# Optimization experiments

Measured on AMD Instinct MI355X. Metric: run time of the kernel, lower is better.

## Reference

```python
import jax, jax.numpy as jnp
import numpy as np

TEMPERATURE = 1.0
EPS = 1e-08


def setup_inputs() -> dict:
    key = jax.random.key(0)
    k1, k2, k3, k4 = jax.random.split(key, 4)
    B, S, D = 4, 4096, 512
    x = jax.random.normal(k1, (B, S, D), dtype=jnp.float32)
    mask = jax.random.randint(k2, (B, S), 0, 2).astype(bool)
    # nn.Linear(dim, dim): weight [out, in], bias [out]
    W = jax.random.normal(k3, (D, D), dtype=jnp.float32) * (1.0 / np.sqrt(D))
    b = jax.random.normal(k4, (D,), dtype=jnp.float32) * 0.01
    return {"x": x, "mask": mask, "W": W, "b": b}


def reference(x, mask, W, b):
    # pairwise squared euclidean distances (cdist p=2, squared)
    sq = jnp.sum(x * x, axis=-1)                                  # [B,S]
    d2 = sq[:, :, None] + sq[:, None, :] - 2.0 * jnp.einsum('bsd,btd->bst', x, x)
    d2 = jnp.maximum(d2, 0.0)                                      # [B,S,S]
    # gaussian kernel: exp(-(sqrt(d2)/T)^2) == exp(-d2/T^2) (avoids sqrt-at-0)
    w = jnp.exp(-d2 / (TEMPERATURE * TEMPERATURE))
    pair_mask = (mask[:, None, :] & mask[:, :, None]).astype(w.dtype)
    w = w * pair_mask
    denom = jnp.maximum(jnp.sum(w, axis=-1, keepdims=True), EPS)
    attn = w / denom                                               # [B,S,S]
    v = jnp.einsum('bsd,ed->bse', x, W) + b                        # [B,S,D]
    return jnp.einsum('bst,btd->bsd', attn, v)
```

## Files before the change

### kernel.cpp

```cpp
#include <hip/hip_runtime.h>
#include <hip/hip_bf16.h>
#include <stdint.h>

#define TB 4
#define TS 4096
#define TD 512
#define TN (TB*TS)

#define KS 64
#define TRI 528
#define D2_THRESH 40.0f
#define EPSV 1e-8f
#define ROW_CAP 16
#define OVF_CAP 32768

typedef unsigned short u16;
typedef unsigned int   u32;
typedef __attribute__((ext_vector_type(8))) short bf16x8;
typedef __attribute__((ext_vector_type(4))) float f32x4;

#define OFF_WH    (33554432u)
#define OFF_WL    (OFF_WH + 524288u)
#define OFF_SQ    (OFF_WL + 524288u)
#define OFF_DEN   (OFF_SQ + 65536u)
#define OFF_RC    (OFF_DEN + 65536u)
#define OFF_OC    (OFF_RC + 65536u)
#define OFF_OVF   (OFF_OC + 256u)
#define OFF_RL    (OFF_OVF + 262144u)
#define OFF_SQ64  (OFF_RL + 1048576u)

__device__ inline u16 b16(float v) {
  __hip_bfloat16 hb = __float2bfloat16(v);
  return *(u16*)&hb;
}
__device__ inline void bsplit(float v, u16& h, u16& l) {
  __hip_bfloat16 hb = __float2bfloat16(v);
  float hf = __bfloat162float(hb);
  __hip_bfloat16 lb = __float2bfloat16(v - hf);
  h = *(u16*)&hb; l = *(u16*)&lb;
}

__device__ inline void gl_lds16(const void* g, void* l) {
  __builtin_amdgcn_global_load_lds(
      (const __attribute__((address_space(1))) u32*)g,
      (__attribute__((address_space(3))) u32*)l, 16, 0, 0);
}

__global__ __launch_bounds__(256) void prep_kernel(
    const float* __restrict__ x, const float* __restrict__ W,
    u16* __restrict__ xb, float* __restrict__ sq, float* __restrict__ sq64,
    u16* __restrict__ Wh, u16* __restrict__ Wl) {
  int bid = blockIdx.x, tid = threadIdx.x;
  if (bid < TN/4) {
    int row  = bid*4 + (tid >> 6);
    int lane = tid & 63;
    const float4* xv = (const float4*)(x + (size_t)row*TD + lane*8);
    float4 a = xv[0], b = xv[1];
    float p = a.x*a.x + a.y*a.y + a.z*a.z + a.w*a.w
            + b.x*b.x + b.y*b.y + b.z*b.z + b.w*b.w;
    if (lane < 8) {
      uint4 pk;
      pk.x = (unsigned)b16(a.x) | ((unsigned)b16(a.y) << 16);
      pk.y = (unsigned)b16(a.z) | ((unsigned)b16(a.w) << 16);
      pk.z = (unsigned)b16(b.x) | ((unsigned)b16(b.y) << 16);
      pk.w = (unsigned)b16(b.z) | ((unsigned)b16(b.w) << 16);
      *(uint4*)(xb + (size_t)row*KS + lane*8) = pk;
    }
    p += __shfl_xor(p, 1); p += __shfl_xor(p, 2); p += __shfl_xor(p, 4);
    float p8 = p;
    p += __shfl_xor(p, 8); p += __shfl_xor(p, 16); p += __shfl_xor(p, 32);
    if (lane == 0) { sq[row] = p; sq64[row] = p8; }
  } else {
    int idx = (bid - TN/4)*256 + tid;
    const float4* wv = (const float4*)(W + (size_t)idx*8);
    float4 a = wv[0], b = wv[1];
    float ev[8] = {a.x,a.y,a.z,a.w,b.x,b.y,b.z,b.w};
    u16 hs[8], ls[8];
    #pragma unroll
    for (int t = 0; t < 8; ++t) bsplit(ev[t], hs[t], ls[t]);
    uint4 hv, lv;
    hv.x = hs[0]|((unsigned)hs[1]<<16); hv.y = hs[2]|((unsigned)hs[3]<<16);
    hv.z = hs[4]|((unsigned)hs[5]<<16); hv.w = hs[6]|((unsigned)hs[7]<<16);
    lv.x = ls[0]|((unsigned)ls[1]<<16); lv.y = ls[2]|((unsigned)ls[3]<<16);
    lv.z = ls[4]|((unsigned)ls[5]<<16); lv.w = ls[6]|((unsigned)ls[7]<<16);
    *(uint4*)(Wh + (size_t)idx*8) = hv;
    *(uint4*)(Wl + (size_t)idx*8) = lv;
  }
}

__device__ inline void append_pair(int gi, int gj, int* rowcnt, int* rowlist,
                                   int2* ovf, int* ovf_cnt) {
  int slot = atomicAdd(&rowcnt[gi], 1);
  if (slot < ROW_CAP) rowlist[gi*ROW_CAP + slot] = gj;
  else { int o = atomicAdd(ovf_cnt, 1); if (o < OVF_CAP) ovf[o] = make_int2(gi, gj); }
}

__global__ __launch_bounds__(256,4) void screen_kernel(
    const u16* __restrict__ xb, const float* __restrict__ sq64,
    const int* __restrict__ mask, int* __restrict__ rowcnt, int* __restrict__ rowlist,
    int2* __restrict__ ovf, int* __restrict__ ovf_cnt) {
  __shared__ __align__(16) u16 lA[128*64];
  __shared__ __align__(16) u16 lB[128*64];
  int bid = blockIdx.x;
  int batch = bid / TRI;
  int t = bid - batch*TRI;
  int ti = (int)((sqrtf(8.0f*t + 1.0f) - 1.0f)*0.5f);
  while ((ti+1)*(ti+2)/2 <= t) ++ti;
  while (ti*(ti+1)/2 > t)      --ti;
  int tj = t - ti*(ti+1)/2;
  int tid = threadIdx.x, lane = tid & 63, w = tid >> 6, wr = w >> 1, wc = w & 1;
  int rowA = batch*TS + ti*128;
  int rowB = batch*TS + tj*128;
  f32x4 zero = {0.f,0.f,0.f,0.f};
  f32x4 acc[4][4];
  #pragma unroll
  for (int m = 0; m < 4; ++m)
    #pragma unroll
    for (int n = 0; n < 4; ++n) acc[m][n] = zero;

  #pragma unroll
  for (int q = 0; q < 4; ++q) {
    int rbase = w*32 + q*8;
    int r  = rbase + (lane >> 3);
    int sg = (lane & 7) ^ (r & 7);
    gl_lds16(xb + (size_t)(rowA + r)*KS + sg*8, &lA[rbase*64]);
    gl_lds16(xb + (size_t)(rowB + r)*KS + sg*8, &lB[rbase*64]);
  }
  __syncthreads();
  #pragma unroll
  for (int kc = 0; kc < 2; ++kc) {
    bf16x8 af[4], bfr[4];
    #pragma unroll
    for (int m = 0; m < 4; ++m) {
      int r = wr*64 + m*16 + (lane & 15);
      int s0 = (lane >> 4) + kc*4;
      af[m] = *(bf16x8*)&lA[r*64 + (s0 ^ (r & 7))*8];
    }
    #pragma unroll
    for (int n = 0; n < 4; ++n) {
      int r = wc*64 + n*16 + (lane & 15);
      int s0 = (lane >> 4) + kc*4;
      bfr[n] = *(bf16x8*)&lB[r*64 + (s0 ^ (r & 7))*8];
    }
    #pragma unroll
    for (int m = 0; m < 4; ++m)
      #pragma unroll
      for (int n = 0; n < 4; ++n)
        acc[m][n] = __builtin_amdgcn_mfma_f32_16x16x32_bf16(af[m], bfr[n], acc[m][n], 0, 0, 0);
  }
  int hi = lane >> 4, lo = lane & 15;
  #pragma unroll
  for (int m = 0; m < 4; ++m) {
    #pragma unroll
    for (int n = 0; n < 4; ++n) {
      #pragma unroll
      for (int r4 = 0; r4 < 4; ++r4) {
        int gi = rowA + wr*64 + m*16 + hi*4 + r4;
        int gj = rowB + wc*64 + n*16 + lo;
        float d2 = sq64[gi] + sq64[gj] - 2.0f*acc[m][n][r4];
        if (d2 <= D2_THRESH && mask[gi] && mask[gj]) {
          append_pair(gi, gj, rowcnt, rowlist, ovf, ovf_cnt);
          if (ti != tj) append_pair(gj, gi, rowcnt, rowlist, ovf, ovf_cnt);
        }
      }
    }
  }
}

__device__ inline void accum_pair(int j, const float* __restrict__ x,
                                  const float* __restrict__ sq, float sqi,
                                  const float4& a0, const float4& a1, int lane,
                                  float acc[8], float& dsum) {
  const float4* xj = (const float4*)(x + (size_t)j*TD + lane*8);
  float4 b0 = xj[0], b1 = xj[1];
  float d = a0.x*b0.x + a0.y*b0.y + a0.z*b0.z + a0.w*b0.w
          + a1.x*b1.x + a1.y*b1.y + a1.z*b1.z + a1.w*b1.w;
  d += __shfl_xor(d, 1); d += __shfl_xor(d, 2); d += __shfl_xor(d, 4);
  d += __shfl_xor(d, 8); d += __shfl_xor(d, 16); d += __shfl_xor(d, 32);
  float d2  = fmaxf(sqi + sq[j] - 2.0f*d, 0.0f);
  float wgt = expf(-d2);
  acc[0] += wgt*b0.x; acc[1] += wgt*b0.y; acc[2] += wgt*b0.z; acc[3] += wgt*b0.w;
  acc[4] += wgt*b1.x; acc[5] += wgt*b1.y; acc[6] += wgt*b1.z; acc[7] += wgt*b1.w;
  dsum += wgt;
}

__global__ __launch_bounds__(256) void row_kernel(
    const float* __restrict__ x, const float* __restrict__ sq,
    const int* __restrict__ rowcnt, const int* __restrict__ rowlist,
    const int2* __restrict__ ovf, const int* __restrict__ ovf_cnt,
    u16* __restrict__ yh, float* __restrict__ den) {
  int i    = blockIdx.x*4 + (threadIdx.x >> 6);
  int lane = threadIdx.x & 63;
  const float4* xi = (const float4*)(x + (size_t)i*TD + lane*8);
  float4 a0 = xi[0], a1 = xi[1];
  float sqi = sq[i];
  float acc[8] = {0.f,0.f,0.f,0.f,0.f,0.f,0.f,0.f};
  float dsum = 0.f;
  int nj = rowcnt[i]; if (nj > ROW_CAP) nj = ROW_CAP;
  for (int t = 0; t < nj; ++t)
    accum_pair(rowlist[i*ROW_CAP + t], x, sq, sqi, a0, a1, lane, acc, dsum);
  int no = *ovf_cnt; if (no > OVF_CAP) no = OVF_CAP;
  for (int t = 0; t < no; ++t) {
    int2 pr = ovf[t];
    if (pr.x == i) accum_pair(pr.y, x, sq, sqi, a0, a1, lane, acc, dsum);
  }
  float inv = 1.0f / fmaxf(dsum, EPSV);
  u16 hs[8];
  #pragma unroll
  for (int e = 0; e < 8; ++e) hs[e] = b16(acc[e]*inv);
  uint4 hv;
  hv.x = hs[0]|((unsigned)hs[1]<<16); hv.y = hs[2]|((unsigned)hs[3]<<16);
  hv.z = hs[4]|((unsigned)hs[5]<<16); hv.w = hs[6]|((unsigned)hs[7]<<16);
  *(uint4*)(yh + (size_t)i*TD + lane*8) = hv;
  if (lane == 0) den[i] = dsum;
}

__global__ __launch_bounds__(256,2) void out_gemm_kernel(
    const u16* __restrict__ yh, const float* __restrict__ den,
    const u16* __restrict__ Wh, const u16* __restrict__ Wl,
    const float* __restrict__ bias, float* __restrict__ out) {
  __shared__ __align__(16) u16 lAh[128*64];
  __shared__ __align__(16) u16 lBh[128*64];
  __shared__ __align__(16) u16 lBl[128*64];
  int mt = blockIdx.x, nt = blockIdx.y;
  int tid = threadIdx.x, lane = tid & 63, w = tid >> 6, wr = w >> 1, wc = w & 1;
  f32x4 zero = {0.f,0.f,0.f,0.f};
  f32x4 acc[4][4];
  #pragma unroll
  for (int m = 0; m < 4; ++m)
    #pragma unroll
    for (int n = 0; n < 4; ++n) acc[m][n] = zero;

  for (int ks = 0; ks < 8; ++ks) {
    int k0 = ks*64;
    #pragma unroll
    for (int q = 0; q < 4; ++q) {
      int rbase = w*32 + q*8;
      int r  = rbase + (lane >> 3);
      int sg = (lane & 7) ^ (r & 7);
      size_t aoff = (size_t)(mt*128 + r)*TD + k0 + sg*8;
      size_t boff = (size_t)(nt*128 + r)*TD + k0 + sg*8;
      gl_lds16(yh + aoff, &lAh[rbase*64]);
      gl_lds16(Wh + boff, &lBh[rbase*64]);
      gl_lds16(Wl + boff, &lBl[rbase*64]);
    }
    __syncthreads();
    #pragma unroll
    for (int kc = 0; kc < 2; ++kc) {
      bf16x8 ah[4], bh[4], bl[4];
      #pragma unroll
      for (int m = 0; m < 4; ++m) {
        int r = wr*64 + m*16 + (lane & 15);
        int s0 = (lane >> 4) + kc*4;
        ah[m] = *(bf16x8*)&lAh[r*64 + (s0 ^ (r & 7))*8];
      }
      #pragma unroll
      for (int n = 0; n < 4; ++n) {
        int r = wc*64 + n*16 + (lane & 15);
        int s0 = (lane >> 4) + kc*4;
        int o = r*64 + (s0 ^ (r & 7))*8;
        bh[n] = *(bf16x8*)&lBh[o];
        bl[n] = *(bf16x8*)&lBl[o];
      }
      #pragma unroll
      for (int m = 0; m < 4; ++m)
        #pragma unroll
        for (int n = 0; n < 4; ++n) {
          acc[m][n] = __builtin_amdgcn_mfma_f32_16x16x32_bf16(ah[m], bh[n], acc[m][n], 0, 0, 0);
          acc[m][n] = __builtin_amdgcn_mfma_f32_16x16x32_bf16(ah[m], bl[n], acc[m][n], 0, 0, 0);
        }
    }
    __syncthreads();
  }
  int hi = lane >> 4, lo = lane & 15;
  #pragma unroll
  for (int m = 0; m < 4; ++m)
    #pragma unroll
    for (int n = 0; n < 4; ++n)
      #pragma unroll
      for (int r4 = 0; r4 < 4; ++r4) {
        int grow = mt*128 + wr*64 + m*16 + hi*4 + r4;
        int col  = nt*128 + wc*64 + n*16 + lo;
        float dn = den[grow];
        float s  = dn / fmaxf(dn, EPSV);
        out[(size_t)grow*TD + col] = acc[m][n][r4] + s*bias[col];
      }
}

extern "C" void kernel_launch(void* const* d_in, const int* in_sizes, int n_in,
                              void* d_out, int out_size, void* d_ws, size_t ws_size,
                              hipStream_t stream) {
  (void)in_sizes; (void)n_in; (void)out_size; (void)ws_size;
  const float* x    = (const float*)d_in[0];
  const int*   mask = (const int*)d_in[1];
  const float* W    = (const float*)d_in[2];
  const float* bias = (const float*)d_in[3];
  float* out = (float*)d_out;
  char*  ws  = (char*)d_ws;

  u16*   xb      = (u16*)(ws + 0);
  u16*   yh      = (u16*)(ws + 0);
  u16*   Wh      = (u16*)(ws + OFF_WH);
  u16*   Wl      = (u16*)(ws + OFF_WL);
  float* sq      = (float*)(ws + OFF_SQ);
  float* den     = (float*)(ws + OFF_DEN);
  int*   rowcnt  = (int*)(ws + OFF_RC);
  int*   ovf_cnt = (int*)(ws + OFF_OC);
  int2*  ovf     = (int2*)(ws + OFF_OVF);
  int*   rowlist = (int*)(ws + OFF_RL);
  float* sq64    = (float*)(ws + OFF_SQ64);

  hipMemsetAsync(rowcnt, 0, 65536 + 256, stream);
  prep_kernel<<<TN/4 + 128, 256, 0, stream>>>(x, W, xb, sq, sq64, Wh, Wl);
  screen_kernel<<<TB*TRI, 256, 0, stream>>>(xb, sq64, mask, rowcnt, rowlist, ovf, ovf_cnt);
  row_kernel<<<TN/4, 256, 0, stream>>>(x, sq, rowcnt, rowlist, ovf, ovf_cnt, yh, den);
  dim3 g(TN/128, TD/128);
  out_gemm_kernel<<<g, 256, 0, stream>>>(yh, den, Wh, Wl, bias, out);
}
```

Measured before the change: 139.7 us.

## Drop W low-part split GEMM, fold mask into sq64, and remove memset

The output GEMM now multiplies by a single bf16 copy of W instead of the high+low split, which halves its MFMAs and its LDS and global traffic for B. That also allows four blocks per CU instead of two. The mask is folded into sq64 as a huge sentinel, so screening no longer reads the mask, and the memset of the counters is merged into prep_kernel. The bias load in the epilogue is hoisted. W now contributes only bf16 precision to the output, which raises error and could matter for tolerance.

```diff
diff --git a/kernel.cpp b/kernel.cpp
--- a/kernel.cpp
+++ b/kernel.cpp
@@ -13,6 +13,7 @@
 #define EPSV 1e-8f
 #define ROW_CAP 16
 #define OVF_CAP 32768
+#define MASKED_SQ 1e30f
 
 typedef unsigned short u16;
 typedef unsigned int   u32;
@@ -33,12 +34,6 @@
   __hip_bfloat16 hb = __float2bfloat16(v);
   return *(u16*)&hb;
 }
-__device__ inline void bsplit(float v, u16& h, u16& l) {
-  __hip_bfloat16 hb = __float2bfloat16(v);
-  float hf = __bfloat162float(hb);
-  __hip_bfloat16 lb = __float2bfloat16(v - hf);
-  h = *(u16*)&hb; l = *(u16*)&lb;
-}
 
 __device__ inline void gl_lds16(const void* g, void* l) {
   __builtin_amdgcn_global_load_lds(
@@ -48,9 +43,11 @@
 
 __global__ __launch_bounds__(256) void prep_kernel(
     const float* __restrict__ x, const float* __restrict__ W,
+    const int* __restrict__ mask,
     u16* __restrict__ xb, float* __restrict__ sq, float* __restrict__ sq64,
-    u16* __restrict__ Wh, u16* __restrict__ Wl) {
+    u16* __restrict__ Wh, int* __restrict__ rowcnt, int* __restrict__ ovf_cnt) {
   int bid = blockIdx.x, tid = threadIdx.x;
+  if (bid == 0 && tid == 0) *ovf_cnt = 0;
   if (bid < TN/4) {
     int row  = bid*4 + (tid >> 6);
     int lane = tid & 63;
@@ -69,22 +66,18 @@
     p += __shfl_xor(p, 1); p += __shfl_xor(p, 2); p += __shfl_xor(p, 4);
     float p8 = p;
     p += __shfl_xor(p, 8); p += __shfl_xor(p, 16); p += __shfl_xor(p, 32);
-    if (lane == 0) { sq[row] = p; sq64[row] = p8; }
+    if (lane == 0) { sq[row] = p; sq64[row] = mask[row] ? p8 : MASKED_SQ; }
+    if (lane == 1) rowcnt[row] = 0;
   } else {
     int idx = (bid - TN/4)*256 + tid;
     const float4* wv = (const float4*)(W + (size_t)idx*8);
     float4 a = wv[0], b = wv[1];
-    float ev[8] = {a.x,a.y,a.z,a.w,b.x,b.y,b.z,b.w};
-    u16 hs[8], ls[8];
-    #pragma unroll
-    for (int t = 0; t < 8; ++t) bsplit(ev[t], hs[t], ls[t]);
-    uint4 hv, lv;
-    hv.x = hs[0]|((unsigned)hs[1]<<16); hv.y = hs[2]|((unsigned)hs[3]<<16);
-    hv.z = hs[4]|((unsigned)hs[5]<<16); hv.w = hs[6]|((unsigned)hs[7]<<16);
-    lv.x = ls[0]|((unsigned)ls[1]<<16); lv.y = ls[2]|((unsigned)ls[3]<<16);
-    lv.z = ls[4]|((unsigned)ls[5]<<16); lv.w = ls[6]|((unsigned)ls[7]<<16);
+    uint4 hv;
+    hv.x = (unsigned)b16(a.x) | ((unsigned)b16(a.y) << 16);
+    hv.y = (unsigned)b16(a.z) | ((unsigned)b16(a.w) << 16);
+    hv.z = (unsigned)b16(b.x) | ((unsigned)b16(b.y) << 16);
+    hv.w = (unsigned)b16(b.z) | ((unsigned)b16(b.w) << 16);
     *(uint4*)(Wh + (size_t)idx*8) = hv;
-    *(uint4*)(Wl + (size_t)idx*8) = lv;
   }
 }
 
@@ -97,7 +90,7 @@
 
 __global__ __launch_bounds__(256,4) void screen_kernel(
     const u16* __restrict__ xb, const float* __restrict__ sq64,
-    const int* __restrict__ mask, int* __restrict__ rowcnt, int* __restrict__ rowlist,
+    int* __restrict__ rowcnt, int* __restrict__ rowlist,
     int2* __restrict__ ovf, int* __restrict__ ovf_cnt) {
   __shared__ __align__(16) u16 lA[128*64];
   __shared__ __align__(16) u16 lB[128*64];
@@ -158,7 +151,7 @@
         int gi = rowA + wr*64 + m*16 + hi*4 + r4;
         int gj = rowB + wc*64 + n*16 + lo;
         float d2 = sq64[gi] + sq64[gj] - 2.0f*acc[m][n][r4];
-        if (d2 <= D2_THRESH && mask[gi] && mask[gj]) {
+        if (d2 <= D2_THRESH) {
           append_pair(gi, gj, rowcnt, rowlist, ovf, ovf_cnt);
           if (ti != tj) append_pair(gj, gi, rowcnt, rowlist, ovf, ovf_cnt);
         }
@@ -215,13 +208,12 @@
   if (lane == 0) den[i] = dsum;
 }
 
-__global__ __launch_bounds__(256,2) void out_gemm_kernel(
+__global__ __launch_bounds__(256,4) void out_gemm_kernel(
     const u16* __restrict__ yh, const float* __restrict__ den,
-    const u16* __restrict__ Wh, const u16* __restrict__ Wl,
-    const float* __restrict__ bias, float* __restrict__ out) {
+    const u16* __restrict__ Wh, const float* __restrict__ bias,
+    float* __restrict__ out) {
   __shared__ __align__(16) u16 lAh[128*64];
   __shared__ __align__(16) u16 lBh[128*64];
-  __shared__ __align__(16) u16 lBl[128*64];
   int mt = blockIdx.x, nt = blockIdx.y;
   int tid = threadIdx.x, lane = tid & 63, w = tid >> 6, wr = w >> 1, wc = w & 1;
   f32x4 zero = {0.f,0.f,0.f,0.f};
@@ -238,16 +230,13 @@
       int rbase = w*32 + q*8;
       int r  = rbase + (lane >> 3);
       int sg = (lane & 7) ^ (r & 7);
-      size_t aoff = (size_t)(mt*128 + r)*TD + k0 + sg*8;
-      size_t boff = (size_t)(nt*128 + r)*TD + k0 + sg*8;
-      gl_lds16(yh + aoff, &lAh[rbase*64]);
-      gl_lds16(Wh + boff, &lBh[rbase*64]);
-      gl_lds16(Wl + boff, &lBl[rbase*64]);
+      gl_lds16(yh + (size_t)(mt*128 + r)*TD + k0 + sg*8, &lAh[rbase*64]);
+      gl_lds16(Wh + (size_t)(nt*128 + r)*TD + k0 + sg*8, &lBh[rbase*64]);
     }
     __syncthreads();
     #pragma unroll
     for (int kc = 0; kc < 2; ++kc) {
-      bf16x8 ah[4], bh[4], bl[4];
+      bf16x8 ah[4], bh[4];
       #pragma unroll
       for (int m = 0; m < 4; ++m) {
         int r = wr*64 + m*16 + (lane & 15);
@@ -258,33 +247,33 @@
       for (int n = 0; n < 4; ++n) {
         int r = wc*64 + n*16 + (lane & 15);
         int s0 = (lane >> 4) + kc*4;
-        int o = r*64 + (s0 ^ (r & 7))*8;
-        bh[n] = *(bf16x8*)&lBh[o];
-        bl[n] = *(bf16x8*)&lBl[o];
+        bh[n] = *(bf16x8*)&lBh[r*64 + (s0 ^ (r & 7))*8];
       }
       #pragma unroll
       for (int m = 0; m < 4; ++m)
         #pragma unroll
-        for (int n = 0; n < 4; ++n) {
+        for (int n = 0; n < 4; ++n)
           acc[m][n] = __builtin_amdgcn_mfma_f32_16x16x32_bf16(ah[m], bh[n], acc[m][n], 0, 0, 0);
-          acc[m][n] = __builtin_amdgcn_mfma_f32_16x16x32_bf16(ah[m], bl[n], acc[m][n], 0, 0, 0);
-        }
     }
     __syncthreads();
   }
   int hi = lane >> 4, lo = lane & 15;
+  float bcol[4];
+  #pragma unroll
+  for (int n = 0; n < 4; ++n) bcol[n] = bias[nt*128 + wc*64 + n*16 + lo];
   #pragma unroll
   for (int m = 0; m < 4; ++m)
     #pragma unroll
-    for (int n = 0; n < 4; ++n)
-      #pragma unroll
-      for (int r4 = 0; r4 < 4; ++r4) {
-        int grow = mt*128 + wr*64 + m*16 + hi*4 + r4;
-        int col  = nt*128 + wc*64 + n*16 + lo;
-        float dn = den[grow];
-        float s  = dn / fmaxf(dn, EPSV);
-        out[(size_t)grow*TD + col] = acc[m][n][r4] + s*bias[col];
+    for (int r4 = 0; r4 < 4; ++r4) {
+      int grow = mt*128 + wr*64 + m*16 + hi*4 + r4;
+      float dn = den[grow];
+      float s  = dn / fmaxf(dn, EPSV);
+      #pragma unroll
+      for (int n = 0; n < 4; ++n) {
+        int col = nt*128 + wc*64 + n*16 + lo;
+        out[(size_t)grow*TD + col] = acc[m][n][r4] + s*bcol[n];
       }
+    }
 }
 
 extern "C" void kernel_launch(void* const* d_in, const int* in_sizes, int n_in,
@@ -301,7 +290,6 @@
   u16*   xb      = (u16*)(ws + 0);
   u16*   yh      = (u16*)(ws + 0);
   u16*   Wh      = (u16*)(ws + OFF_WH);
-  u16*   Wl      = (u16*)(ws + OFF_WL);
   float* sq      = (float*)(ws + OFF_SQ);
   float* den     = (float*)(ws + OFF_DEN);
   int*   rowcnt  = (int*)(ws + OFF_RC);
@@ -310,10 +298,9 @@
   int*   rowlist = (int*)(ws + OFF_RL);
   float* sq64    = (float*)(ws + OFF_SQ64);
 
-  hipMemsetAsync(rowcnt, 0, 65536 + 256, stream);
-  prep_kernel<<<TN/4 + 128, 256, 0, stream>>>(x, W, xb, sq, sq64, Wh, Wl);
-  screen_kernel<<<TB*TRI, 256, 0, stream>>>(xb, sq64, mask, rowcnt, rowlist, ovf, ovf_cnt);
+  prep_kernel<<<TN/4 + 128, 256, 0, stream>>>(x, W, mask, xb, sq, sq64, Wh, rowcnt, ovf_cnt);
+  screen_kernel<<<TB*TRI, 256, 0, stream>>>(xb, sq64, rowcnt, rowlist, ovf, ovf_cnt);
   row_kernel<<<TN/4, 256, 0, stream>>>(x, sq, rowcnt, rowlist, ovf, ovf_cnt, yh, den);
   dim3 g(TN/128, TD/128);
-  out_gemm_kernel<<<g, 256, 0, stream>>>(yh, den, Wh, Wl, bias, out);
-}
+  out_gemm_kernel<<<g, 256, 0, stream>>>(yh, den, Wh, bias, out);
+}
```

Result: faster. 132.7 us (-5.0%).
